# Kernel tuning notes

Hardware: AMD Instinct MI355X
Metric: run time of the kernel (lower is better)

## Reference

```python
import jax, jax.numpy as jnp
import numpy as np

G, N, F_IN = 1024, 256, 128
HID = [256, 256, 256]
KS = [32, 16, 8]
N_OUT = 2


def _graph_conv(adj, x, W, b, act):
    # DGL GraphConv, norm='both': h = D^{-1/2} A D^{-1/2} X W + b
    deg = adj.sum(-1)                                   # [G, n]
    norm = jax.lax.rsqrt(jnp.maximum(deg, 1.0))[..., None]
    h = (x * norm) @ W                                  # [G, n, d_out]
    h = jnp.einsum('gnm,gmd->gnd', adj, h) * norm + b
    return act(h) if act is not None else h


def _sag_pool(adj, x, Ws, bs, k):
    # SAGPool: score via GraphConv, keep top-k nodes, gate by tanh(score),
    # take induced subgraph adjacency.
    score = _graph_conv(adj, x, Ws, bs, None)[..., 0]   # [G, n]
    sv, idx = jax.lax.top_k(score, k)                   # [G, k]
    x_sel = jnp.take_along_axis(x, idx[:, :, None], axis=1) * jnp.tanh(sv)[:, :, None]
    a = jnp.take_along_axis(adj, idx[:, :, None], axis=1)
    a = jnp.take_along_axis(a, idx[:, None, :], axis=2)  # [G, k, k]
    return a, x_sel


def _sum_max_readout(x):
    return jnp.concatenate([x.sum(axis=1), x.max(axis=1)], axis=-1)  # [G, 2d]


def setup_inputs() -> dict:
    key = jax.random.key(0)
    ks = jax.random.split(key, 16)
    feat = jax.random.normal(ks[0], (G, N, F_IN), dtype=jnp.float32)
    # sparse-ish symmetric binary adjacency, avg degree ~ 16
    a = (jax.random.uniform(ks[1], (G, N, N)) < (16.0 / N)).astype(jnp.float32)
    adj = jnp.maximum(a, jnp.swapaxes(a, 1, 2))

    def glorot(k, shp):
        lim = float(np.sqrt(6.0 / (shp[0] + shp[1])))
        return jax.random.uniform(k, shp, jnp.float32, -lim, lim)

    dims = [F_IN] + HID
    inp = {'feat': feat, 'adj': adj}
    for i in range(3):
        inp[f'W{i}'] = glorot(ks[2 + i], (dims[i], dims[i + 1]))
        inp[f'b{i}'] = jnp.zeros((dims[i + 1],), jnp.float32)
        inp[f'Ws{i}'] = glorot(ks[5 + i], (dims[i + 1], 1))
        inp[f'bs{i}'] = jnp.zeros((1,), jnp.float32)
    inp['Wd1'] = glorot(ks[8], (2 * sum(HID), 128))
    inp['bd1'] = jnp.zeros((128,), jnp.float32)
    inp['Wd2'] = glorot(ks[9], (128, N_OUT))
    inp['bd2'] = jnp.zeros((N_OUT,), jnp.float32)
    return inp


def reference(feat, adj, W0, b0, Ws0, bs0, W1, b1, Ws1, bs1, W2, b2, Ws2, bs2,
              Wd1, bd1, Wd2, bd2):
    act = jax.nn.leaky_relu  # F.leaky_relu, slope 0.01
    Wgs = [(W0, b0), (W1, b1), (W2, b2)]
    Wss = [(Ws0, bs0), (Ws1, bs1), (Ws2, bs2)]
    readouts = []
    x, a = feat, adj
    for i in range(3):
        x = _graph_conv(a, x, Wgs[i][0], Wgs[i][1], act)
        a, x = _sag_pool(a, x, Wss[i][0], Wss[i][1], KS[i])
        readouts.append(_sum_max_readout(x))
    merged = jnp.concatenate(readouts, axis=1)          # [G, 2*sum(HID)]
    # dropout omitted (deterministic eval reference)
    h = act(merged @ Wd1 + bd1)
    out = jax.nn.sigmoid(h @ Wd2 + bd2)                 # [G, n_output]
    return out
```

## Files before the change

### kernel.cpp

```cpp
#include <hip/hip_runtime.h>
#include <math.h>

constexpr int GG  = 1024;
constexpr int NN  = 256;
constexpr int FF  = 128;
constexpr int DD  = 256;
constexpr int KS0 = 32, KS1 = 16, KS2 = 8;

__device__ __forceinline__ float lrelu(float x){ return x >= 0.f ? x : 0.01f*x; }

__device__ __forceinline__ unsigned short f2bf(float f) {
  unsigned u = __float_as_uint(f);
  unsigned r = (u + 0x7FFFu + ((u >> 16) & 1u)) >> 16;
  return (unsigned short)r;
}
__device__ __forceinline__ float bf2f(unsigned short h) {
  return __uint_as_float(((unsigned)h) << 16);
}

typedef __attribute__((ext_vector_type(8)))  __bf16 bf16x8;
typedef __attribute__((ext_vector_type(16))) float  f32x16;

union Frag8 { unsigned short us[8]; unsigned long long u64[2]; bf16x8 v; };

__global__ void k_splitW_all(const float* __restrict__ Wa, const float* __restrict__ Wb,
                             const float* __restrict__ Wc,
                             unsigned short* __restrict__ oa, unsigned short* __restrict__ ob,
                             unsigned short* __restrict__ oc) {
  int e = blockIdx.x*256 + threadIdx.x;
  if (e >= FF*DD + 2*DD*DD) return;
  const float* W; unsigned short* out; int K;
  if (e < FF*DD)                { W = Wa; out = oa; K = FF; }
  else if (e < FF*DD + DD*DD)   { e -= FF*DD; W = Wb; out = ob; K = DD; }
  else                          { e -= FF*DD + DD*DD; W = Wc; out = oc; K = DD; }
  int j    = e & 7;
  int lane = (e >> 3) & 63;
  int nt   = (e >> 9) & 7;
  int s    = (e >> 12) & 1;
  int kti  = e >> 13;
  int n = nt*32 + (lane & 31);
  int k = kti*32 + s*16 + ((lane >> 5) << 3) + j;
  float x = W[(size_t)k*DD + n];
  unsigned short h1 = f2bf(x);  float r1 = x - bf2f(h1);
  unsigned short h2 = f2bf(r1); float r2 = r1 - bf2f(h2);
  unsigned short h3 = f2bf(r2);
  out[e] = h1; out[DD*K + e] = h2; out[2*DD*K + e] = h3;
}

__global__ void k_maskrow(const float* __restrict__ adj, float* __restrict__ norm0,
                          unsigned long long* __restrict__ mask) {
  int row = blockIdx.x*4 + (threadIdx.x >> 6);
  int lane = threadIdx.x & 63;
  const float* ar = adj + (size_t)row*NN;
  float f0 = ar[lane], f1 = ar[64 + lane], f2 = ar[128 + lane], f3 = ar[192 + lane];
  unsigned long long m0 = __ballot(f0 > 0.5f);
  unsigned long long m1 = __ballot(f1 > 0.5f);
  unsigned long long m2 = __ballot(f2 > 0.5f);
  unsigned long long m3 = __ballot(f3 > 0.5f);
  if (lane < 4) {
    unsigned long long mm = lane == 0 ? m0 : lane == 1 ? m1 : lane == 2 ? m2 : m3;
    mask[(size_t)row*4 + lane] = mm;
  }
  if (lane == 0) {
    int cnt = __popcll(m0) + __popcll(m1) + __popcll(m2) + __popcll(m3);
    norm0[row] = rsqrtf(fmaxf((float)cnt, 1.0f));
  }
}

__global__ __launch_bounds__(256, 4) void k_spmm_s(
    const float* __restrict__ feat, const unsigned long long* __restrict__ mask,
    const float* __restrict__ norm0, float* __restrict__ T0) {
  constexpr int ST = 36;
  __shared__ float ls[NN*ST];
  __shared__ float snorm[NN];
  int bid = blockIdx.x;
  int g = bid >> 2, q = bid & 3;
  int t = threadIdx.x;
  const float* Xg = feat + (size_t)g*NN*FF + q*32;

  snorm[t] = norm0[g*NN + t];
  const unsigned long long* mp = mask + ((size_t)g*NN + t)*4;
  unsigned long long mrow[4];
  #pragma unroll
  for (int w = 0; w < 4; ++w) mrow[w] = mp[w];
  __syncthreads();

  #pragma unroll
  for (int i = 0; i < 8; ++i) {
    int e = t + i*256;
    int r = e >> 3, c4 = (e & 7)*4;
    float4 v = *reinterpret_cast<const float4*>(Xg + (size_t)r*FF + c4);
    float nv = snorm[r];
    v.x *= nv; v.y *= nv; v.z *= nv; v.w *= nv;
    *reinterpret_cast<float4*>(&ls[r*ST + c4]) = v;
  }
  __syncthreads();

  float4 acc[8];
  #pragma unroll
  for (int i = 0; i < 8; ++i) acc[i] = make_float4(0.f, 0.f, 0.f, 0.f);
  #pragma unroll
  for (int w = 0; w < 4; ++w) {
    unsigned long long m = mrow[w];
    while (m) {
      int c = __builtin_ctzll(m);
      const float4* xp = reinterpret_cast<const float4*>(&ls[(w*64 + c)*ST]);
      #pragma unroll
      for (int i = 0; i < 8; ++i) {
        float4 v = xp[i];
        acc[i].x += v.x; acc[i].y += v.y; acc[i].z += v.z; acc[i].w += v.w;
      }
      m &= m - 1;
    }
  }
  float* op = T0 + ((size_t)g*NN + t)*FF + q*32;
  #pragma unroll
  for (int i = 0; i < 8; ++i)
    *reinterpret_cast<float4*>(op + i*4) = acc[i];
}

__global__ __launch_bounds__(256, 2) void k_gemm0(
    const float* __restrict__ Tmat, const unsigned short* __restrict__ Wk,
    const float* __restrict__ normv, const float* __restrict__ bias,
    const float* __restrict__ Ws, float* __restrict__ hs) {
  int t = threadIdx.x;
  int lane = t & 63, wave = t >> 6;
  int lm = lane & 31, lh = lane >> 5;
  int rowbase = blockIdx.x*128 + wave*32;

  f32x16 acc[8];
  #pragma unroll
  for (int nt = 0; nt < 8; ++nt) acc[nt] = (f32x16)0.0f;

  for (int kti = 0; kti < 4; ++kti) {
    int kt = kti*32;
    float4 af[2][2];
    #pragma unroll
    for (int s = 0; s < 2; ++s) {
      const float* ap = Tmat + (size_t)(rowbase + lm)*FF + kt + s*16 + lh*8;
      af[s][0] = *reinterpret_cast<const float4*>(ap);
      af[s][1] = *reinterpret_cast<const float4*>(ap + 4);
    }
    Frag8 afr[2][3];
    #pragma unroll
    for (int s = 0; s < 2; ++s) {
      const float* fv = &af[s][0].x;
      #pragma unroll
      for (int j = 0; j < 8; ++j) {
        float x = fv[j];
        unsigned short h1 = f2bf(x);  float r1 = x - bf2f(h1);
        unsigned short h2 = f2bf(r1); float r2 = r1 - bf2f(h2);
        afr[s][0].us[j] = h1; afr[s][1].us[j] = h2; afr[s][2].us[j] = f2bf(r2);
      }
    }
    #pragma unroll
    for (int s = 0; s < 2; ++s)
      #pragma unroll
      for (int nt = 0; nt < 8; ++nt) {
        size_t boff = ((((size_t)kti*2 + s)*8 + nt)*64 + lane)*8;
        Frag8 b0_, b1_, b2_;
        b0_.v = *reinterpret_cast<const bf16x8*>(Wk + boff);
        b1_.v = *reinterpret_cast<const bf16x8*>(Wk + (size_t)DD*FF + boff);
        b2_.v = *reinterpret_cast<const bf16x8*>(Wk + (size_t)2*DD*FF + boff);
        acc[nt] = __builtin_amdgcn_mfma_f32_32x32x16_bf16(afr[s][0].v, b0_.v, acc[nt], 0,0,0);
        acc[nt] = __builtin_amdgcn_mfma_f32_32x32x16_bf16(afr[s][0].v, b1_.v, acc[nt], 0,0,0);
        acc[nt] = __builtin_amdgcn_mfma_f32_32x32x16_bf16(afr[s][1].v, b0_.v, acc[nt], 0,0,0);
        acc[nt] = __builtin_amdgcn_mfma_f32_32x32x16_bf16(afr[s][0].v, b2_.v, acc[nt], 0,0,0);
        acc[nt] = __builtin_amdgcn_mfma_f32_32x32x16_bf16(afr[s][2].v, b0_.v, acc[nt], 0,0,0);
        acc[nt] = __builtin_amdgcn_mfma_f32_32x32x16_bf16(afr[s][1].v, b1_.v, acc[nt], 0,0,0);
      }
  }

  float bcol[8], wcol[8];
  #pragma unroll
  for (int nt = 0; nt < 8; ++nt) { int col = nt*32 + lm; bcol[nt] = bias[col]; wcol[nt] = Ws[col]; }
  float hsum[16];
  #pragma unroll
  for (int r = 0; r < 16; ++r) {
    int row = rowbase + (r & 3) + 8*(r >> 2) + 4*lh;
    float nv = normv[row];
    float hp = 0.f;
    #pragma unroll
    for (int nt = 0; nt < 8; ++nt) hp += lrelu(nv*acc[nt][r] + bcol[nt])*wcol[nt];
    hsum[r] = hp;
  }
  #pragma unroll
  for (int off = 1; off <= 16; off <<= 1)
    #pragma unroll
    for (int r = 0; r < 16; ++r) hsum[r] += __shfl_xor(hsum[r], off);
  if (lm == 0)
    #pragma unroll
    for (int r = 0; r < 16; ++r) {
      int row = rowbase + (r & 3) + 8*(r >> 2) + 4*lh;
      hs[row] = normv[row]*hsum[r];
    }
}

__global__ __launch_bounds__(256) void k_topk_sel0(
    const unsigned long long* __restrict__ mask, const float* __restrict__ hs,
    const float* __restrict__ norm0, const float* __restrict__ bs,
    const float* __restrict__ T0, const float* __restrict__ W0,
    const float* __restrict__ b0, float* __restrict__ x_sel,
    float* __restrict__ a1, float* __restrict__ merged) {
  __shared__ float sh[NN];
  __shared__ float ssc[NN];
  __shared__ float sT[KS0*FF];
  __shared__ int sidx[KS0]; __shared__ float stv[KS0]; __shared__ float snv[KS0];
  int g = blockIdx.x, t = threadIdx.x;

  sh[t] = hs[g*NN + t];
  __syncthreads();
  const unsigned long long* mr = mask + ((size_t)g*NN + t)*4;
  float s = 0.f;
  #pragma unroll
  for (int w = 0; w < 4; ++w) {
    unsigned long long m = mr[w];
    const float* base = sh + w*64;
    while (m) {
      int c = __builtin_ctzll(m);
      s += base[c];
      m &= m - 1;
    }
  }
  ssc[t] = norm0[g*NN + t]*s + bs[0];
  __syncthreads();
  if (t < 64) {
    float sv[4]; int si[4];
    #pragma unroll
    for (int e = 0; e < 4; ++e) { sv[e] = ssc[e*64 + t]; si[e] = e*64 + t; }
    for (int kk = 0; kk < KS0; ++kk) {
      float bs_ = -INFINITY; int bi = 1 << 30;
      #pragma unroll
      for (int e = 0; e < 4; ++e)
        if (sv[e] > bs_ || (sv[e] == bs_ && si[e] < bi)) { bs_ = sv[e]; bi = si[e]; }
      for (int off = 32; off; off >>= 1) {
        float os = __shfl_xor(bs_, off);
        int oi = __shfl_xor(bi, off);
        if (os > bs_ || (os == bs_ && oi < bi)) { bs_ = os; bi = oi; }
      }
      if (t == 0) { sidx[kk] = bi; stv[kk] = tanhf(bs_); }
      #pragma unroll
      for (int e = 0; e < 4; ++e) if (si[e] == bi) sv[e] = -INFINITY;
    }
  }
  __syncthreads();
  if (t < KS0) snv[t] = norm0[g*NN + sidx[t]];
  #pragma unroll
  for (int i = 0; i < 4; ++i) {
    int e4 = t + i*256;
    int r = e4 >> 5, c4 = e4 & 31;
    reinterpret_cast<float4*>(sT)[e4] =
        *reinterpret_cast<const float4*>(&T0[((size_t)g*NN + sidx[r])*FF + c4*4]);
  }
  __syncthreads();
  float sum[KS0];
  #pragma unroll
  for (int j = 0; j < KS0; ++j) sum[j] = 0.f;
  for (int k = 0; k < FF; k += 4) {
    float4 w;
    w.x = W0[(size_t)(k+0)*DD + t]; w.y = W0[(size_t)(k+1)*DD + t];
    w.z = W0[(size_t)(k+2)*DD + t]; w.w = W0[(size_t)(k+3)*DD + t];
    #pragma unroll
    for (int j = 0; j < KS0; ++j) {
      float4 tv4 = *reinterpret_cast<const float4*>(&sT[j*FF + k]);
      sum[j] += tv4.x*w.x + tv4.y*w.y + tv4.z*w.z + tv4.w*w.w;
    }
  }
  float b = b0[t];
  float ssum = 0.f, mx = -INFINITY;
  #pragma unroll
  for (int j = 0; j < KS0; ++j) {
    float val = lrelu(snv[j]*sum[j] + b) * stv[j];
    x_sel[((size_t)g*KS0 + j)*DD + t] = val;
    ssum += val; mx = fmaxf(mx, val);
  }
  merged[(size_t)g*1536 + t] = ssum;
  merged[(size_t)g*1536 + 256 + t] = mx;
  for (int e = t; e < KS0*KS0; e += 256) {
    int r = e >> 5, c = e & 31;
    int nr = sidx[r], nc = sidx[c];
    unsigned long long m = mask[((size_t)g*NN + nr)*4 + (nc >> 6)];
    a1[(size_t)g*KS0*KS0 + e] = (float)((m >> (nc & 63)) & 1ull);
  }
}

__global__ __launch_bounds__(256, 2) void k_fused1(
    const float* __restrict__ a, const float* __restrict__ xin,
    const unsigned short* __restrict__ Wk, const float* __restrict__ bias,
    const float* __restrict__ Ws, const float* __restrict__ bs,
    float* __restrict__ x_sel_out, float* __restrict__ a_out,
    float* __restrict__ merged) {
  constexpr int n = KS0;
  constexpr int kp = KS1;
  constexpr int TP = DD + 4;
  __shared__ float sa[n*n];
  __shared__ float bufA[n*DD];
  __shared__ float sT[n*TP];
  __shared__ float snorm[n]; __shared__ float shs[n]; __shared__ float ssc[n];
  __shared__ int sidx[kp]; __shared__ float stv[kp];
  int g = blockIdx.x, t = threadIdx.x;
  int lane = t & 63, wave = t >> 6, lm = lane & 31, lh = lane >> 5;

  for (int e = t; e < n*n; e += 256) sa[e] = a[(size_t)g*n*n + e];
  __syncthreads();
  if (t < n) {
    float dg = 0.f;
    for (int m = 0; m < n; ++m) dg += sa[m*n + t];
    snorm[t] = rsqrtf(fmaxf(dg, 1.f));
  }
  __syncthreads();
  {
    const float4* xp = reinterpret_cast<const float4*>(xin + (size_t)g*n*DD);
    #pragma unroll
    for (int i = 0; i < (n*DD/4)/256; ++i) {
      int e4 = t + i*256;
      float4 v = xp[e4];
      float nv = snorm[e4 >> 6];
      v.x *= nv; v.y *= nv; v.z *= nv; v.w *= nv;
      reinterpret_cast<float4*>(bufA)[e4] = v;
    }
  }
  __syncthreads();
  {
    float acc2[n];
    #pragma unroll
    for (int r = 0; r < n; ++r) acc2[r] = 0.f;
    for (int m = 0; m < n; ++m) {
      float xv = bufA[m*DD + t];
      #pragma unroll
      for (int r = 0; r < n; ++r) acc2[r] += sa[r*n + m]*xv;
    }
    #pragma unroll
    for (int r = 0; r < n; ++r) sT[r*TP + t] = acc2[r];
  }
  __syncthreads();

  f32x16 acc[2];
  acc[0] = (f32x16)0.0f; acc[1] = (f32x16)0.0f;
  for (int kti = 0; kti < DD/32; ++kti) {
    int kt = kti*32;
    Frag8 afr[2][3];
    #pragma unroll
    for (int s = 0; s < 2; ++s) {
      float4 af4[2];
      const float* ap = &sT[lm*TP + kt + s*16 + lh*8];
      af4[0] = *reinterpret_cast<const float4*>(ap);
      af4[1] = *reinterpret_cast<const float4*>(ap + 4);
      const float* fv = &af4[0].x;
      #pragma unroll
      for (int j = 0; j < 8; ++j) {
        float x = fv[j];
        unsigned short h1 = f2bf(x);  float r1 = x - bf2f(h1);
        unsigned short h2 = f2bf(r1); float r2 = r1 - bf2f(h2);
        afr[s][0].us[j] = h1; afr[s][1].us[j] = h2; afr[s][2].us[j] = f2bf(r2);
      }
    }
    #pragma unroll
    for (int s = 0; s < 2; ++s)
      #pragma unroll
      for (int ntl = 0; ntl < 2; ++ntl) {
        int ct = wave*2 + ntl;
        size_t boff = ((((size_t)kti*2 + s)*8 + ct)*64 + lane)*8;
        Frag8 b0_, b1_, b2_;
        b0_.v = *reinterpret_cast<const bf16x8*>(Wk + boff);
        b1_.v = *reinterpret_cast<const bf16x8*>(Wk + (size_t)DD*DD + boff);
        b2_.v = *reinterpret_cast<const bf16x8*>(Wk + (size_t)2*DD*DD + boff);
        acc[ntl] = __builtin_amdgcn_mfma_f32_32x32x16_bf16(afr[s][0].v, b0_.v, acc[ntl], 0,0,0);
        acc[ntl] = __builtin_amdgcn_mfma_f32_32x32x16_bf16(afr[s][0].v, b1_.v, acc[ntl], 0,0,0);
        acc[ntl] = __builtin_amdgcn_mfma_f32_32x32x16_bf16(afr[s][1].v, b0_.v, acc[ntl], 0,0,0);
        acc[ntl] = __builtin_amdgcn_mfma_f32_32x32x16_bf16(afr[s][0].v, b2_.v, acc[ntl], 0,0,0);
        acc[ntl] = __builtin_amdgcn_mfma_f32_32x32x16_bf16(afr[s][2].v, b0_.v, acc[ntl], 0,0,0);
        acc[ntl] = __builtin_amdgcn_mfma_f32_32x32x16_bf16(afr[s][1].v, b1_.v, acc[ntl], 0,0,0);
      }
  }

  #pragma unroll
  for (int ntl = 0; ntl < 2; ++ntl) {
    int colbase = wave*64 + ntl*32 + lm;
    float bc = bias[colbase];
    #pragma unroll
    for (int r = 0; r < 16; ++r) {
      int row = (r & 3) + 8*(r >> 2) + 4*lh;
      bufA[row*DD + colbase] = lrelu(snorm[row]*acc[ntl][r] + bc);
    }
  }
  __syncthreads();
  if (wave == 0) {
    float wcol[8];
    #pragma unroll
    for (int nt = 0; nt < 8; ++nt) wcol[nt] = Ws[nt*32 + lm];
    float hsum[16];
    #pragma unroll
    for (int r = 0; r < 16; ++r) {
      int row = (r & 3) + 8*(r >> 2) + 4*lh;
      float hp = 0.f;
      #pragma unroll
      for (int nt = 0; nt < 8; ++nt) hp += bufA[row*DD + nt*32 + lm]*wcol[nt];
      hsum[r] = hp;
    }
    #pragma unroll
    for (int off = 1; off <= 16; off <<= 1)
      #pragma unroll
      for (int r = 0; r < 16; ++r) hsum[r] += __shfl_xor(hsum[r], off);
    if (lm == 0)
      #pragma unroll
      for (int r = 0; r < 16; ++r) {
        int row = (r & 3) + 8*(r >> 2) + 4*lh;
        shs[row] = snorm[row]*hsum[r];
      }
  }
  __syncthreads();
  if (t < n) {
    float s = 0.f;
    for (int m = 0; m < n; ++m) s += sa[m*n + t]*shs[m];
    ssc[t] = snorm[t]*s + bs[0];
  }
  __syncthreads();
  if (t < 64) {
    float sc = (t < n) ? ssc[t] : -INFINITY;
    int si = (t < n) ? t : (1 << 30);
    for (int kk = 0; kk < kp; ++kk) {
      float bs_ = sc; int bi = si;
      for (int off = 32; off; off >>= 1) {
        float os = __shfl_xor(bs_, off);
        int oi = __shfl_xor(bi, off);
        if (os > bs_ || (os == bs_ && oi < bi)) { bs_ = os; bi = oi; }
      }
      if (t == 0) { sidx[kk] = bi; stv[kk] = tanhf(bs_); }
      if (si == bi) sc = -INFINITY;
    }
  }
  __syncthreads();
  float sum = 0.f, mx = -INFINITY;
  #pragma unroll
  for (int j = 0; j < kp; ++j) {
    float v = bufA[sidx[j]*DD + t] * stv[j];
    x_sel_out[((size_t)g*kp + j)*DD + t] = v;
    sum += v; mx = fmaxf(mx, v);
  }
  merged[(size_t)g*1536 + 512 + t] = sum;
  merged[(size_t)g*1536 + 768 + t] = mx;
  { int r = t >> 4, c = t & 15;
    a_out[(size_t)g*kp*kp + t] = sa[sidx[r]*n + sidx[c]]; }
}

__global__ __launch_bounds__(256, 2) void k_fused2(
    const float* __restrict__ a, const float* __restrict__ xin,
    const unsigned short* __restrict__ Wk, const float* __restrict__ bias,
    const float* __restrict__ Ws, const float* __restrict__ bs,
    float* __restrict__ merged) {
  constexpr int n = KS1;
  constexpr int kp = KS2;
  constexpr int TP = DD + 4;
  __shared__ float sa[n*n];
  __shared__ float bufA[n*DD];
  __shared__ float sT[n*TP];
  __shared__ float snorm[n]; __shared__ float shs[n]; __shared__ float ssc[n];
  __shared__ int sidx[kp]; __shared__ float stv[kp];
  int g = blockIdx.x, t = threadIdx.x;
  int lane = t & 63, wave = t >> 6, lm = lane & 31, lh = lane >> 5;

  for (int e = t; e < n*n; e += 256) sa[e] = a[(size_t)g*n*n + e];
  __syncthreads();
  if (t < n) {
    float dg = 0.f;
    for (int m = 0; m < n; ++m) dg += sa[m*n + t];
    snorm[t] = rsqrtf(fmaxf(dg, 1.f));
  }
  __syncthreads();
  {
    const float4* xp = reinterpret_cast<const float4*>(xin + (size_t)g*n*DD);
    #pragma unroll
    for (int i = 0; i < (n*DD/4)/256; ++i) {
      int e4 = t + i*256;
      float4 v = xp[e4];
      float nv = snorm[e4 >> 6];
      v.x *= nv; v.y *= nv; v.z *= nv; v.w *= nv;
      reinterpret_cast<float4*>(bufA)[e4] = v;
    }
  }
  __syncthreads();
  {
    float acc2[n];
    #pragma unroll
    for (int r = 0; r < n; ++r) acc2[r] = 0.f;
    for (int m = 0; m < n; ++m) {
      float xv = bufA[m*DD + t];
      #pragma unroll
      for (int r = 0; r < n; ++r) acc2[r] += sa[r*n + m]*xv;
    }
    #pragma unroll
    for (int r = 0; r < n; ++r) sT[r*TP + t] = acc2[r];
  }
  __syncthreads();

  f32x16 acc[2];
  acc[0] = (f32x16)0.0f; acc[1] = (f32x16)0.0f;
  for (int kti = 0; kti < DD/32; ++kti) {
    int kt = kti*32;
    Frag8 afr[2][3];
    #pragma unroll
    for (int s = 0; s < 2; ++s) {
      float4 af4[2];
      if (lm < n) {
        const float* ap = &sT[lm*TP + kt + s*16 + lh*8];
        af4[0] = *reinterpret_cast<const float4*>(ap);
        af4[1] = *reinterpret_cast<const float4*>(ap + 4);
      } else {
        af4[0] = make_float4(0.f, 0.f, 0.f, 0.f);
        af4[1] = make_float4(0.f, 0.f, 0.f, 0.f);
      }
      const float* fv = &af4[0].x;
      #pragma unroll
      for (int j = 0; j < 8; ++j) {
        float x = fv[j];
        unsigned short h1 = f2bf(x);  float r1 = x - bf2f(h1);
        unsigned short h2 = f2bf(r1); float r2 = r1 - bf2f(h2);
        afr[s][0].us[j] = h1; afr[s][1].us[j] = h2; afr[s][2].us[j] = f2bf(r2);
      }
    }
    #pragma unroll
    for (int s = 0; s < 2; ++s)
      #pragma unroll
      for (int ntl = 0; ntl < 2; ++ntl) {
        int ct = wave*2 + ntl;
        size_t boff = ((((size_t)kti*2 + s)*8 + ct)*64 + lane)*8;
        Frag8 b0_, b1_, b2_;
        b0_.v = *reinterpret_cast<const bf16x8*>(Wk + boff);
        b1_.v = *reinterpret_cast<const bf16x8*>(Wk + (size_t)DD*DD + boff);
        b2_.v = *reinterpret_cast<const bf16x8*>(Wk + (size_t)2*DD*DD + boff);
        acc[ntl] = __builtin_amdgcn_mfma_f32_32x32x16_bf16(afr[s][0].v, b0_.v, acc[ntl], 0,0,0);
        acc[ntl] = __builtin_amdgcn_mfma_f32_32x32x16_bf16(afr[s][0].v, b1_.v, acc[ntl], 0,0,0);
        acc[ntl] = __builtin_amdgcn_mfma_f32_32x32x16_bf16(afr[s][1].v, b0_.v, acc[ntl], 0,0,0);
        acc[ntl] = __builtin_amdgcn_mfma_f32_32x32x16_bf16(afr[s][0].v, b2_.v, acc[ntl], 0,0,0);
        acc[ntl] = __builtin_amdgcn_mfma_f32_32x32x16_bf16(afr[s][2].v, b0_.v, acc[ntl], 0,0,0);
        acc[ntl] = __builtin_amdgcn_mfma_f32_32x32x16_bf16(afr[s][1].v, b1_.v, acc[ntl], 0,0,0);
      }
  }

  #pragma unroll
  for (int ntl = 0; ntl < 2; ++ntl) {
    int colbase = wave*64 + ntl*32 + lm;
    float bc = bias[colbase];
    #pragma unroll
    for (int r = 0; r < 16; ++r) {
      int row = (r & 3) + 8*(r >> 2) + 4*lh;
      if (row < n) bufA[row*DD + colbase] = lrelu(snorm[row]*acc[ntl][r] + bc);
    }
  }
  __syncthreads();
  if (wave == 0) {
    float wcol[8];
    #pragma unroll
    for (int nt = 0; nt < 8; ++nt) wcol[nt] = Ws[nt*32 + lm];
    float hsum[16];
    #pragma unroll
    for (int r = 0; r < 16; ++r) {
      int row = (r & 3) + 8*(r >> 2) + 4*lh;
      float hp = 0.f;
      if (row < n) {
        #pragma unroll
        for (int nt = 0; nt < 8; ++nt) hp += bufA[row*DD + nt*32 + lm]*wcol[nt];
      }
      hsum[r] = hp;
    }
    #pragma unroll
    for (int off = 1; off <= 16; off <<= 1)
      #pragma unroll
      for (int r = 0; r < 16; ++r) hsum[r] += __shfl_xor(hsum[r], off);
    if (lm == 0)
      #pragma unroll
      for (int r = 0; r < 16; ++r) {
        int row = (r & 3) + 8*(r >> 2) + 4*lh;
        if (row < n) shs[row] = snorm[row]*hsum[r];
      }
  }
  __syncthreads();
  if (t < n) {
    float s = 0.f;
    for (int m = 0; m < n; ++m) s += sa[m*n + t]*shs[m];
    ssc[t] = snorm[t]*s + bs[0];
  }
  __syncthreads();
  if (t < 64) {
    float sc = (t < n) ? ssc[t] : -INFINITY;
    int si = (t < n) ? t : (1 << 30);
    for (int kk = 0; kk < kp; ++kk) {
      float bs_ = sc; int bi = si;
      for (int off = 32; off; off >>= 1) {
        float os = __shfl_xor(bs_, off);
        int oi = __shfl_xor(bi, off);
        if (os > bs_ || (os == bs_ && oi < bi)) { bs_ = os; bi = oi; }
      }
      if (t == 0) { sidx[kk] = bi; stv[kk] = tanhf(bs_); }
      if (si == bi) sc = -INFINITY;
    }
  }
  __syncthreads();
  float sum = 0.f, mx = -INFINITY;
  #pragma unroll
  for (int j = 0; j < kp; ++j) {
    float v = bufA[sidx[j]*DD + t] * stv[j];
    sum += v; mx = fmaxf(mx, v);
  }
  merged[(size_t)g*1536 + 1024 + t] = sum;
  merged[(size_t)g*1536 + 1280 + t] = mx;
}

__global__ void k_mlp(const float* __restrict__ merged, const float* __restrict__ Wd1,
                      const float* __restrict__ bd1, const float* __restrict__ Wd2,
                      const float* __restrict__ bd2, float* __restrict__ out) {
  __shared__ float sm[4*1536];
  __shared__ float sh[4][128];
  int g0 = blockIdx.x*4; int t = threadIdx.x;
  for (int i = t; i < 4*1536; i += 128) sm[i] = merged[(size_t)g0*1536 + i];
  __syncthreads();
  float a0 = 0.f, a1 = 0.f, a2 = 0.f, a3 = 0.f;
  for (int kk = 0; kk < 1536; ++kk) {
    float w = Wd1[(size_t)kk*128 + t];
    a0 += sm[kk]*w; a1 += sm[1536 + kk]*w; a2 += sm[3072 + kk]*w; a3 += sm[4608 + kk]*w;
  }
  float b = bd1[t];
  sh[0][t] = lrelu(a0 + b); sh[1][t] = lrelu(a1 + b);
  sh[2][t] = lrelu(a2 + b); sh[3][t] = lrelu(a3 + b);
  __syncthreads();
  if (t < 8) {
    int gi = t >> 1, c = t & 1;
    float o = 0.f;
    for (int kk = 0; kk < 128; ++kk) o += sh[gi][kk]*Wd2[kk*2 + c];
    out[(size_t)(g0 + gi)*2 + c] = 1.f/(1.f + expf(-(o + bd2[c])));
  }
}

extern "C" void kernel_launch(void* const* d_in, const int* in_sizes, int n_in,
                              void* d_out, int out_size, void* d_ws, size_t ws_size,
                              hipStream_t stream) {
  const float* feat = (const float*)d_in[0];
  const float* adj  = (const float*)d_in[1];
  const float* W0 = (const float*)d_in[2];  const float* b0  = (const float*)d_in[3];
  const float* Ws0= (const float*)d_in[4];  const float* bs0 = (const float*)d_in[5];
  const float* W1 = (const float*)d_in[6];  const float* b1  = (const float*)d_in[7];
  const float* Ws1= (const float*)d_in[8];  const float* bs1 = (const float*)d_in[9];
  const float* W2 = (const float*)d_in[10]; const float* b2  = (const float*)d_in[11];
  const float* Ws2= (const float*)d_in[12]; const float* bs2 = (const float*)d_in[13];
  const float* Wd1= (const float*)d_in[14]; const float* bd1 = (const float*)d_in[15];
  const float* Wd2= (const float*)d_in[16]; const float* bd2 = (const float*)d_in[17];
  float* out = (float*)d_out;

  char* ws = (char*)d_ws;
  size_t off = 0;
  auto alloc = [&](size_t bytes) -> char* {
    char* p = ws + off; off += (bytes + 255) & ~(size_t)255; return p;
  };
  float* norm0 = (float*)alloc((size_t)GG*NN*4);
  unsigned long long* mask0 = (unsigned long long*)alloc((size_t)GG*NN*4*8);
  float* hs0   = (float*)alloc((size_t)GG*NN*4);
  float* merged= (float*)alloc((size_t)GG*1536*4);
  unsigned short* W0s = (unsigned short*)alloc((size_t)3*FF*DD*2);
  unsigned short* W1s = (unsigned short*)alloc((size_t)3*DD*DD*2);
  unsigned short* W2s = (unsigned short*)alloc((size_t)3*DD*DD*2);
  float* T0     = (float*)alloc((size_t)GG*NN*FF*4);
  float* x_sel1 = (float*)alloc((size_t)GG*KS0*DD*4);
  float* a1     = (float*)alloc((size_t)GG*KS0*KS0*4);
  float* x_sel2 = (float*)alloc((size_t)GG*KS1*DD*4);
  float* a2     = (float*)alloc((size_t)GG*KS1*KS1*4);

  k_splitW_all<<<(FF*DD + 2*DD*DD)/256, 256, 0, stream>>>(W0, W1, W2, W0s, W1s, W2s);

  k_maskrow<<<GG*NN/4, 256, 0, stream>>>(adj, norm0, mask0);
  k_spmm_s<<<4*GG, 256, 0, stream>>>(feat, mask0, norm0, T0);
  k_gemm0<<<GG*NN/128, 256, 0, stream>>>(T0, W0s, norm0, b0, Ws0, hs0);
  k_topk_sel0<<<GG, 256, 0, stream>>>(mask0, hs0, norm0, bs0, T0, W0, b0, x_sel1, a1, merged);

  k_fused1<<<GG, 256, 0, stream>>>(a1, x_sel1, W1s, b1, Ws1, bs1, x_sel2, a2, merged);

  k_fused2<<<GG, 256, 0, stream>>>(a2, x_sel2, W2s, b2, Ws2, bs2, merged);

  k_mlp<<<GG/4, 128, 0, stream>>>(merged, Wd1, bd1, Wd2, bd2, out);

  (void)in_sizes; (void)n_in; (void)out_size; (void)ws_size;
}
```

Baseline: 927.6 us.

## Sort rows by degree in sparse aggregation to balance wavefront work

In the first-layer sparse aggregation kernel, each block now builds a shared-memory histogram of row degrees, prefix-sums it, and permutes rows so threads in a wavefront process rows of similar degree. The goal is to cut divergence in the per-row bit-iteration loop, where a wavefront waits for its slowest lane. Results are written back through shared memory in the original row order so global stores stay coalesced. This adds several barriers, LDS atomics, a reload of the mask rows, and an extra staging pass through shared memory.

```diff
diff --git a/kernel.cpp b/kernel.cpp
--- a/kernel.cpp
+++ b/kernel.cpp
@@ -78,12 +78,43 @@
   int t = threadIdx.x;
   const float* Xg = feat + (size_t)g*NN*FF + q*32;
 
-  snorm[t] = norm0[g*NN + t];
-  const unsigned long long* mp = mask + ((size_t)g*NN + t)*4;
-  unsigned long long mrow[4];
-  #pragma unroll
-  for (int w = 0; w < 4; ++w) mrow[w] = mp[w];
-  __syncthreads();
+  int* hist = reinterpret_cast<int*>(ls);
+  int* bs   = hist + 256;
+  int* prm  = hist + 512;
+  {
+    const unsigned long long* mp = mask + ((size_t)g*NN + t)*4;
+    unsigned long long m0 = mp[0], m1 = mp[1], m2 = mp[2], m3 = mp[3];
+    int deg = __popcll(m0) + __popcll(m1) + __popcll(m2) + __popcll(m3);
+    snorm[t] = norm0[g*NN + t];
+    hist[t] = 0;
+    __syncthreads();
+    atomicAdd(&hist[deg], 1);
+    __syncthreads();
+    if (t < 64) {
+      int h0 = hist[4*t], h1 = hist[4*t+1], h2 = hist[4*t+2], h3 = hist[4*t+3];
+      int s = h0 + h1 + h2 + h3;
+      int incl = s;
+      #pragma unroll
+      for (int off = 1; off < 64; off <<= 1) {
+        int o = __shfl_up(incl, off);
+        if (t >= off) incl += o;
+      }
+      int excl = incl - s;
+      bs[4*t]   = excl;
+      bs[4*t+1] = excl + h0;
+      bs[4*t+2] = excl + h0 + h1;
+      bs[4*t+3] = excl + h0 + h1 + h2;
+    }
+    __syncthreads();
+    int old = atomicSub(&hist[deg], 1);
+    prm[bs[deg] + old - 1] = t;
+  }
+  __syncthreads();
+  int row = prm[t];
+  __syncthreads();
+
+  const unsigned long long* mr = mask + ((size_t)g*NN + row)*4;
+  unsigned long long n0 = mr[0], n1 = mr[1], n2 = mr[2], n3 = mr[3];
 
   #pragma unroll
   for (int i = 0; i < 8; ++i) {
@@ -101,7 +132,7 @@
   for (int i = 0; i < 8; ++i) acc[i] = make_float4(0.f, 0.f, 0.f, 0.f);
   #pragma unroll
   for (int w = 0; w < 4; ++w) {
-    unsigned long long m = mrow[w];
+    unsigned long long m = w == 0 ? n0 : w == 1 ? n1 : w == 2 ? n2 : n3;
     while (m) {
       int c = __builtin_ctzll(m);
       const float4* xp = reinterpret_cast<const float4*>(&ls[(w*64 + c)*ST]);
@@ -113,10 +144,16 @@
       m &= m - 1;
     }
   }
+  __syncthreads();
+
+  #pragma unroll
+  for (int i = 0; i < 8; ++i)
+    *reinterpret_cast<float4*>(&ls[row*ST + i*4]) = acc[i];
+  __syncthreads();
   float* op = T0 + ((size_t)g*NN + t)*FF + q*32;
   #pragma unroll
   for (int i = 0; i < 8; ++i)
-    *reinterpret_cast<float4*>(op + i*4) = acc[i];
+    *reinterpret_cast<float4*>(op + i*4) = *reinterpret_cast<const float4*>(&ls[t*ST + i*4]);
 }
 
 __global__ __launch_bounds__(256, 2) void k_gemm0(
```

Measured after the change: 929.1 us. No clear change (+0.2%).
